# Kernel optimization log

Hardware: AMD Instinct MI355X
Metric: run time of the kernel (lower is better)

The kernel has to match this reference:

```python
import jax, jax.numpy as jnp
import numpy as np

B, T, D, H = 4, 2048, 1024, 16
HD = D // H  # head_dim = 64
MIX = 0.05   # cross-state coupling coefficient


def setup_inputs() -> dict:
    key = jax.random.key(0)
    ks = jax.random.split(key, 10)
    s = 0.02  # init scale for stability
    return {
        "x": jax.random.normal(ks[0], (B, T, D), jnp.float32),
        "Wq": jax.random.normal(ks[1], (D, D), jnp.float32) * s,
        "Wk": jax.random.normal(ks[2], (D, D), jnp.float32) * s,
        "Wv": jax.random.normal(ks[3], (D, D), jnp.float32) * s,
        "Wo": jax.random.normal(ks[4], (D, D), jnp.float32) * s,
        "Wb": jax.random.normal(ks[5], (H, D), jnp.float32) * s,
        "Wfd": jax.random.normal(ks[6], (H, D), jnp.float32) * s,
        "bfd": jnp.zeros((H,), jnp.float32),
        "Wsd": jax.random.normal(ks[7], (H, D), jnp.float32) * s,
        "bsd": jnp.zeros((H,), jnp.float32),
        "Wg": jax.random.normal(ks[8], (D, D), jnp.float32) * s,
    }


def _deltanet_forward(x, Wq, Wk, Wv, Wo, Wb, Wfd, bfd, Wsd, bsd, Wg):
    b, t, dm = x.shape
    # projections (nn.Linear: x @ W.T)
    def heads(W):  # [B,T,D] -> [B,H,T,hd]
        return (x @ W.T).reshape(b, t, H, HD).transpose(0, 2, 1, 3)
    q = jax.nn.silu(heads(Wq))
    k = jax.nn.silu(heads(Wk))
    v = jax.nn.silu(heads(Wv))
    beta = jax.nn.sigmoid(x @ Wb.T).transpose(0, 2, 1)               # [B,H,T]
    fd = jax.nn.sigmoid(x @ Wfd.T + bfd).transpose(0, 2, 1)          # [B,H,T]
    sd = jax.nn.sigmoid(x @ Wsd.T + bsd).transpose(0, 2, 1)          # [B,H,T]

    # time-major xs for scan
    qT = jnp.moveaxis(q, 2, 0)   # [T,B,H,hd]
    kT = jnp.moveaxis(k, 2, 0)
    vT = jnp.moveaxis(v, 2, 0)
    bT = jnp.moveaxis(beta, 2, 0)  # [T,B,H]
    fT = jnp.moveaxis(fd, 2, 0)
    sT = jnp.moveaxis(sd, 2, 0)

    def step(carry, inp):
        Sf, Ss = carry                       # each [B,H,hd]
        qt, kt, vt, bt, ft, st = inp
        Sf = Sf * ft[..., None]
        Ss = Ss * st[..., None]
        o = 0.5 * qt * (Sf + Ss)             # output before update
        upd = bt[..., None] * kt * vt
        Sf = Sf + upd
        Ss = Ss + upd
        Sf_new = Sf + MIX * Ss
        Ss = Ss + MIX * Sf                   # uses pre-mix Sf
        return (Sf_new, Ss), o

    S0 = jnp.zeros((b, H, HD), x.dtype)
    _, oT = jax.lax.scan(step, (S0, S0), (qT, kT, vT, bT, fT, sT))
    o = jnp.moveaxis(oT, 0, 2)               # [B,H,T,hd]
    o = o.transpose(0, 2, 1, 3).reshape(b, t, dm)  # [B,T,D]
    g = jax.nn.sigmoid(x @ Wg.T)
    return (o * g) @ Wo.T


def reference(x, Wq, Wk, Wv, Wo, Wb, Wfd, bfd, Wsd, bsd, Wg):
    return _deltanet_forward(x, Wq, Wk, Wv, Wo, Wb, Wfd, bfd, Wsd, bsd, Wg)
```

## Files before the change

### kernel.cpp

```cpp
#include <hip/hip_runtime.h>
#include <hip/hip_bf16.h>
#include <stdint.h>

#define BB 4
#define TT 2048
#define DD 1024
#define HH 16
#define MTOK (BB*TT)
#define NQ 4096
#define NW (NQ+128)
#define TC 32
#define NC (TT/TC)
#define BH (BB*HH)
#define ROWT (16*NQ)

typedef __bf16 bf16x8 __attribute__((ext_vector_type(8)));
typedef float f32x4 __attribute__((ext_vector_type(4)));

__device__ __forceinline__ uint16_t f2bf(float f){
  uint32_t u = __float_as_uint(f);
  u += 0x7fffu + ((u >> 16) & 1u);
  return (uint16_t)(u >> 16);
}
__device__ __forceinline__ float bf2f(uint32_t h){ return __uint_as_float(h << 16); }
__device__ __forceinline__ float sigm(float z){
  return __builtin_amdgcn_rcpf(1.f + __expf(-z));
}

__device__ __forceinline__ void gll16(const uint16_t* src, uint16_t* dst){
  __builtin_amdgcn_global_load_lds(
      (const __attribute__((address_space(1))) void*)src,
      (__attribute__((address_space(3))) void*)dst, 16, 0, 0);
}
__device__ __forceinline__ float bfel(const uint4& v, int e){
  uint32_t wrd = ((e>>1)==0) ? v.x : ((e>>1)==1) ? v.y : ((e>>1)==2) ? v.z : v.w;
  return bf2f((e&1) ? (wrd >> 16) : (wrd & 0xffffu));
}

__global__ __launch_bounds__(256) void prep_kernel(
    const float* __restrict__ x,
    const float* __restrict__ Wq, const float* __restrict__ Wk,
    const float* __restrict__ Wv, const float* __restrict__ Wg,
    const float* __restrict__ Wo,
    const float* __restrict__ Wb, const float* __restrict__ Wfd,
    const float* __restrict__ Wsd,
    uint16_t* __restrict__ wcat, uint16_t* __restrict__ wob,
    uint16_t* __restrict__ xb)
{
  const int bx = blockIdx.x;
  if (bx < 5120){
    int i = bx * 256 + threadIdx.x;
    int wsel = i >> 18;
    int loc = i & 262143;
    const float* src = (wsel == 0) ? Wq : (wsel == 1) ? Wk : (wsel == 2) ? Wv : (wsel == 3) ? Wg : Wo;
    uint16_t* dst = (wsel < 4) ? (wcat + (size_t)wsel * DD * DD) : wob;
    float4 v = ((const float4*)src)[loc];
    ushort4 o;
    o.x = f2bf(v.x); o.y = f2bf(v.y); o.z = f2bf(v.z); o.w = f2bf(v.w);
    ((ushort4*)dst)[loc] = o;
  } else if (bx < 9216){
    int base = (bx - 5120) * 512 + threadIdx.x;
    #pragma unroll
    for (int rep = 0; rep < 2; rep++){
      int loc = base + rep * 256;
      float4 v = ((const float4*)x)[loc];
      ushort4 o;
      o.x = f2bf(v.x); o.y = f2bf(v.y); o.z = f2bf(v.z); o.w = f2bf(v.w);
      ((ushort4*)xb)[loc] = o;
    }
  } else {
    int u = (bx - 9216) * 256 + threadIdx.x;
    int row = u >> 8;
    int cidx = (u & 255) * 4;
    ushort4 o = {0, 0, 0, 0};
    if (row < 48){
      const float* src = (row < 16) ? (Wb + (size_t)row * DD)
                       : (row < 32) ? (Wfd + (size_t)(row - 16) * DD)
                                    : (Wsd + (size_t)(row - 32) * DD);
      float4 v = *(const float4*)(src + cidx);
      o.x = f2bf(v.x); o.y = f2bf(v.y); o.z = f2bf(v.z); o.w = f2bf(v.w);
    }
    *(ushort4*)(wcat + (size_t)(NQ + row) * DD + cidx) = o;
  }
}

template<int MODE>
__global__ __launch_bounds__(256) void gemm128(
    const uint16_t* __restrict__ X, const uint16_t* __restrict__ W,
    uint16_t* __restrict__ Y, float* __restrict__ Yf,
    const float* __restrict__ bfd, const float* __restrict__ bsd,
    float* __restrict__ scp, int N, int K)
{
  __shared__ __align__(16) uint16_t lA[128 * 64];
  __shared__ __align__(16) uint16_t lB[128 * 64];
  const int tid = threadIdx.x;
  const int m0 = blockIdx.y * 128, n0 = blockIdx.x * 128;
  const int l = tid & 63, w = tid >> 6;
  const int wr = w >> 1, wc = w & 1;
  const int g = l >> 4, r16 = l & 15;

  const uint16_t* srcA[4];
  const uint16_t* srcB[4];
  uint16_t* dstA[4];
  uint16_t* dstB[4];
  #pragma unroll
  for (int n = 0; n < 4; n++){
    int p = n * 256 + tid;
    int row = p >> 3;
    int cq = (p & 7) ^ (row & 7);
    srcA[n] = X + (size_t)(m0 + row) * K + cq * 8;
    srcB[n] = W + (size_t)(n0 + row) * K + cq * 8;
    int basechunk = n * 256 + (tid & ~63);
    dstA[n] = lA + basechunk * 8;
    dstB[n] = lB + basechunk * 8;
  }

  int roA[4][2], roB[4][2];
  #pragma unroll
  for (int i = 0; i < 4; i++)
    #pragma unroll
    for (int ks = 0; ks < 2; ks++){
      roA[i][ks] = (wr * 64 + i * 16 + r16) * 64 + ((ks * 4 + g) ^ (r16 & 7)) * 8;
      roB[i][ks] = (wc * 64 + i * 16 + r16) * 64 + ((ks * 4 + g) ^ (r16 & 7)) * 8;
    }

  const bool doMfma = (MODE != 2) || (wc == 0);
  const int nLim = (MODE == 2) ? 3 : 4;

  f32x4 acc[4][4];
  #pragma unroll
  for (int i = 0; i < 4; i++)
    #pragma unroll
    for (int j = 0; j < 4; j++) acc[i][j] = (f32x4){0.f, 0.f, 0.f, 0.f};

  for (int kt = 0; kt < K; kt += 64){
    __syncthreads();
    #pragma unroll
    for (int n = 0; n < 4; n++){
      gll16(srcA[n] + kt, dstA[n]);
      gll16(srcB[n] + kt, dstB[n]);
    }
    __syncthreads();

    if (doMfma){
      #pragma unroll
      for (int ks = 0; ks < 2; ks++){
        bf16x8 af[4], bw[4];
        #pragma unroll
        for (int mi = 0; mi < 4; mi++) af[mi] = *(const bf16x8*)(lA + roA[mi][ks]);
        #pragma unroll
        for (int ni = 0; ni < nLim; ni++) bw[ni] = *(const bf16x8*)(lB + roB[ni][ks]);
        #pragma unroll
        for (int mi = 0; mi < 4; mi++)
          #pragma unroll
          for (int ni = 0; ni < nLim; ni++)
            acc[mi][ni] = __builtin_amdgcn_mfma_f32_16x16x32_bf16(af[mi], bw[ni], acc[mi][ni], 0, 0, 0);
      }
    }
  }

  if (MODE == 0){
    const bool dosig = (n0 >= 3 * DD);
    #pragma unroll
    for (int mi = 0; mi < 4; mi++){
      const int R0 = m0 + wr * 64 + mi * 16;
      const size_t rbase = (size_t)(R0 >> 4) * ROWT;
      #pragma unroll
      for (int ni = 0; ni < 4; ni++){
        const int C0 = n0 + wc * 64 + ni * 16;
        f32x4 v = acc[mi][ni];
        float o[4];
        #pragma unroll
        for (int r = 0; r < 4; r++){
          float xx = v[r];
          o[r] = dosig ? sigm(xx) : xx * sigm(xx);
        }
        uint2 pk;
        pk.x = (uint32_t)f2bf(o[0]) | ((uint32_t)f2bf(o[1]) << 16);
        pk.y = (uint32_t)f2bf(o[2]) | ((uint32_t)f2bf(o[3]) << 16);
        size_t off = rbase + (size_t)(C0 >> 4) * 256 + (size_t)r16 * 16 + g * 4;
        *(uint2*)(Y + off) = pk;
      }
    }
  } else if (MODE == 1){
    #pragma unroll
    for (int mi = 0; mi < 4; mi++){
      #pragma unroll
      for (int ni = 0; ni < 4; ni++){
        int rg = m0 + wr * 64 + mi * 16 + g * 4;
        int cg = n0 + wc * 64 + ni * 16 + r16;
        #pragma unroll
        for (int r = 0; r < 4; r++)
          Yf[(size_t)(rg + r) * N + cg] = acc[mi][ni][r];
      }
    }
  } else {
    if (wc == 0){
      #pragma unroll
      for (int ni = 0; ni < 3; ni++){
        const int grp = ni;
        const int h = r16;
        const float bias = (grp == 0) ? 0.f : (grp == 1) ? bfd[h] : bsd[h];
        #pragma unroll
        for (int mi = 0; mi < 4; mi++){
          const int R0 = m0 + wr * 64 + mi * 16 + g * 4;
          const int b = R0 >> 11, t = R0 & (TT - 1);
          f32x4 v = acc[mi][ni];
          float4 o;
          o.x = sigm(v[0] + bias);
          o.y = sigm(v[1] + bias);
          o.z = sigm(v[2] + bias);
          o.w = sigm(v[3] + bias);
          *(float4*)(scp + (((size_t)grp * BB + b) * HH + h) * TT + t) = o;
        }
      }
    }
  }
}


__global__ __launch_bounds__(64) void scan_partA(
    const uint16_t* __restrict__ qkvg, const float* __restrict__ sc,
    float* __restrict__ Lst, float4* __restrict__ Pm)
{
  int j = blockIdx.x, bh = blockIdx.y;
  int b = bh >> 4, h = bh & 15;
  int c = threadIdx.x;
  const int ci = c & 15;
  const size_t tc_k = (size_t)((DD     + h * 64 + c) >> 4) * 256 + ci * 16;
  const size_t tc_v = (size_t)((2 * DD + h * 64 + c) >> 4) * 256 + ci * 16;
  const float* bet = sc + ((size_t)(0 * BB + b) * HH + h) * TT + j * TC;
  const float* fdp = sc + ((size_t)(1 * BB + b) * HH + h) * TT + j * TC;
  const float* sdp = sc + ((size_t)(2 * BB + b) * HH + h) * TT + j * TC;

  float sf = 0.f, ss = 0.f;
  float p00 = 1.f, p01 = 0.f, p10 = 0.f, p11 = 1.f;
  #pragma unroll
  for (int t16 = 0; t16 < 2; ++t16){
    int R0 = b * TT + j * TC + t16 * 16;
    size_t tb = (size_t)(R0 >> 4) * ROWT;
    uint4 kl = *(const uint4*)(qkvg + tb + tc_k);
    uint4 kh = *(const uint4*)(qkvg + tb + tc_k + 8);
    uint4 vl = *(const uint4*)(qkvg + tb + tc_v);
    uint4 vh = *(const uint4*)(qkvg + tb + tc_v + 8);
    const float* bt = bet + t16 * 16;
    const float* ft = fdp + t16 * 16;
    const float* st = sdp + t16 * 16;
    #pragma unroll
    for (int u = 0; u < 16; ++u){
      float kv = (u < 8) ? bfel(kl, u) : bfel(kh, u - 8);
      float vv = (u < 8) ? bfel(vl, u) : bfel(vh, u - 8);
      float btv = bt[u], f = ft[u], s = st[u];
      float uu = 1.05f * btv * kv * vv;
      float bq = 0.05f * s, cq = 0.05f * f;
      float nf = f * sf + bq * ss + uu;
      float ns = cq * sf + s * ss + uu;
      sf = nf; ss = ns;
      float q00 = f * p00 + bq * p10, q01 = f * p01 + bq * p11;
      float q10 = cq * p00 + s * p10, q11 = cq * p01 + s * p11;
      p00 = q00; p01 = q01; p10 = q10; p11 = q11;
    }
  }
  size_t base = ((size_t)bh * NC + j) * 2;
  Lst[(base + 0) * 64 + c] = sf;
  Lst[(base + 1) * 64 + c] = ss;
  if (c == 0) Pm[(size_t)bh * NC + j] = make_float4(p00, p01, p10, p11);
}

__global__ __launch_bounds__(64) void scan_partC(
    const uint16_t* __restrict__ qkvg, const float* __restrict__ sc,
    const float* __restrict__ Lst, const float4* __restrict__ Pm,
    uint16_t* __restrict__ og)
{
  __shared__ uint16_t ot[16 * 64];
  int j = blockIdx.x, bh = blockIdx.y;
  int b = bh >> 4, h = bh & 15;
  int c = threadIdx.x;
  const int ci = c & 15;

  float sf = 0.f, ss = 0.f;
  for (int i = 0; i < j; ++i){
    size_t pbase = ((size_t)bh * NC + i) * 2;
    float lf = Lst[(pbase + 0) * 64 + c];
    float ls = Lst[(pbase + 1) * 64 + c];
    float4 P = Pm[(size_t)bh * NC + i];
    float nf = P.x * sf + P.y * ss + lf;
    float ns = P.z * sf + P.w * ss + ls;
    sf = nf; ss = ns;
  }

  const size_t tc_q = (size_t)((         h * 64 + c) >> 4) * 256 + ci * 16;
  const size_t tc_k = (size_t)((DD     + h * 64 + c) >> 4) * 256 + ci * 16;
  const size_t tc_v = (size_t)((2 * DD + h * 64 + c) >> 4) * 256 + ci * 16;
  const size_t tc_g = (size_t)((3 * DD + h * 64 + c) >> 4) * 256 + ci * 16;
  const float* bet = sc + ((size_t)(0 * BB + b) * HH + h) * TT + j * TC;
  const float* fdp = sc + ((size_t)(1 * BB + b) * HH + h) * TT + j * TC;
  const float* sdp = sc + ((size_t)(2 * BB + b) * HH + h) * TT + j * TC;

  #pragma unroll
  for (int t16 = 0; t16 < 2; ++t16){
    int R0 = b * TT + j * TC + t16 * 16;
    size_t tb = (size_t)(R0 >> 4) * ROWT;
    uint4 ql = *(const uint4*)(qkvg + tb + tc_q);
    uint4 qh = *(const uint4*)(qkvg + tb + tc_q + 8);
    uint4 kl = *(const uint4*)(qkvg + tb + tc_k);
    uint4 kh = *(const uint4*)(qkvg + tb + tc_k + 8);
    uint4 vl = *(const uint4*)(qkvg + tb + tc_v);
    uint4 vh = *(const uint4*)(qkvg + tb + tc_v + 8);
    uint4 gl = *(const uint4*)(qkvg + tb + tc_g);
    uint4 gh = *(const uint4*)(qkvg + tb + tc_g + 8);
    const float* bt = bet + t16 * 16;
    const float* ft = fdp + t16 * 16;
    const float* st = sdp + t16 * 16;
    #pragma unroll
    for (int u = 0; u < 16; ++u){
      float qv = (u < 8) ? bfel(ql, u) : bfel(qh, u - 8);
      float kv = (u < 8) ? bfel(kl, u) : bfel(kh, u - 8);
      float vv = (u < 8) ? bfel(vl, u) : bfel(vh, u - 8);
      float gv = (u < 8) ? bfel(gl, u) : bfel(gh, u - 8);
      float btv = bt[u], f = ft[u], s = st[u];
      sf *= f; ss *= s;
      float o = 0.5f * qv * (sf + ss);
      float uu = btv * kv * vv;
      sf += uu; ss += uu;
      float nf = sf + 0.05f * ss, ns = ss + 0.05f * sf;
      sf = nf; ss = ns;
      ot[u * 64 + c] = f2bf(o * gv);
    }
    __syncthreads();
    {
      int u0 = c >> 3, c8 = c & 7;
      uint4 d0 = *(const uint4*)&ot[u0 * 64 + c8 * 8];
      uint4 d1 = *(const uint4*)&ot[(u0 + 8) * 64 + c8 * 8];
      uint16_t* ob = og + (size_t)R0 * DD + h * 64 + c8 * 8;
      *(uint4*)(ob + (size_t)u0 * DD) = d0;
      *(uint4*)(ob + (size_t)(u0 + 8) * DD) = d1;
    }
    __syncthreads();
  }
}

extern "C" void kernel_launch(void* const* d_in, const int* in_sizes, int n_in,
                              void* d_out, int out_size, void* d_ws, size_t ws_size,
                              hipStream_t stream)
{
  const float* x   = (const float*)d_in[0];
  const float* Wq  = (const float*)d_in[1];
  const float* Wk  = (const float*)d_in[2];
  const float* Wv  = (const float*)d_in[3];
  const float* Wo  = (const float*)d_in[4];
  const float* Wb  = (const float*)d_in[5];
  const float* Wfd = (const float*)d_in[6];
  const float* bfd = (const float*)d_in[7];
  const float* Wsd = (const float*)d_in[8];
  const float* bsd = (const float*)d_in[9];
  const float* Wg  = (const float*)d_in[10];
  float* out = (float*)d_out;

  char* ws = (char*)d_ws;
  size_t off = 0;
  auto alloc = [&](size_t bytes) -> void* {
    void* p = ws + off;
    off += (bytes + 255) & ~(size_t)255;
    return p;
  };

  uint16_t* xb   = (uint16_t*)alloc((size_t)MTOK * DD * 2);
  uint16_t* wcat = (uint16_t*)alloc((size_t)NW * DD * 2);
  uint16_t* wob  = (uint16_t*)alloc((size_t)DD * DD * 2);
  uint16_t* qkvg = (uint16_t*)alloc((size_t)MTOK * NQ * 2);
  float*    sc   = (float*)alloc((size_t)3 * BB * HH * TT * 4);
  float*    Lst  = (float*)alloc((size_t)BH * NC * 2 * 64 * 4);
  float4*   Pm   = (float4*)alloc((size_t)BH * NC * 16);
  uint16_t* ogb  = xb;

  prep_kernel<<<9344, 256, 0, stream>>>(
      x, Wq, Wk, Wv, Wg, Wo, Wb, Wfd, Wsd, wcat, wob, xb);

  dim3 gp(1, MTOK / 128);
  gemm128<2><<<gp, 256, 0, stream>>>(xb, wcat + (size_t)NQ * DD, nullptr, nullptr,
                                     bfd, bsd, sc, NQ, DD);

  dim3 gq(NQ / 128, MTOK / 128);
  gemm128<0><<<gq, 256, 0, stream>>>(xb, wcat, qkvg, nullptr, bfd, bsd, nullptr, NQ, DD);

  dim3 gs(NC, BH);
  scan_partA<<<gs, 64, 0, stream>>>(qkvg, sc, Lst, Pm);
  scan_partC<<<gs, 64, 0, stream>>>(qkvg, sc, Lst, Pm, ogb);

  dim3 go(DD / 128, MTOK / 128);
  gemm128<1><<<go, 256, 0, stream>>>(ogb, wob, nullptr, out, bfd, bsd, nullptr, DD, DD);
}
```

Baseline: 170.8 us.

## Replace QKVG projection GEMM with 256x256-tile, 8-wave, double-buffered pipelined kernel

Adds a dedicated QKVG GEMM kernel using 256x256 output tiles with 512 threads and an 8x4 MFMA accumulator tile per wave. The K loop double-buffers LDS via direct global-to-LDS loads, splits each k-step into half-tiles interleaved with barriers, and raises wave priority around the MFMA bursts so loads overlap compute. This targets the largest GEMM (8192x4096x1024) by improving operand reuse and hiding load latency. The cost is heavy register pressure (128 accumulator floats per lane) and 128 KB of LDS per block, which limits occupancy. Only 512 blocks are launched, so the wave count across the device is small.

```diff
diff --git a/kernel.cpp b/kernel.cpp
--- a/kernel.cpp
+++ b/kernel.cpp
@@ -84,6 +84,155 @@
   }
 }
 
+__global__ __launch_bounds__(512, 2) void gemm256_qkvg(
+    const uint16_t* __restrict__ X, const uint16_t* __restrict__ W,
+    uint16_t* __restrict__ Y)
+{
+  constexpr int K = DD;
+  constexpr int NT = K / 64;
+  constexpr int HSZ = 8192;
+  __shared__ __align__(16) uint16_t sA[2][2][HSZ];
+  __shared__ __align__(16) uint16_t sB[2][2][HSZ];
+
+  const int tid = threadIdx.x;
+  const int m0 = blockIdx.y * 256, n0 = blockIdx.x * 256;
+  const int l = tid & 63, w = tid >> 6;
+  const int wr = w >> 2, wc = w & 3;
+  const int g = l >> 4, r16 = l & 15;
+
+  const int c1 = tid + 512;
+  const int r0 = tid >> 2, q0 = (tid & 3) ^ ((tid >> 3) & 3);
+  const int r1 = c1 >> 2,  q1 = (c1 & 3) ^ ((c1 >> 3) & 3);
+  const uint16_t* pA0 = X + (size_t)(m0 + r0) * K + q0 * 8;
+  const uint16_t* pA1 = X + (size_t)(m0 + r1) * K + q1 * 8;
+  const uint16_t* pB0 = W + (size_t)(n0 + r0) * K + q0 * 8;
+  const uint16_t* pB1 = W + (size_t)(n0 + r1) * K + q1 * 8;
+  const int d0 = w * 512, d1 = 4096 + w * 512;
+
+  const int fsw = (g ^ ((r16 >> 1) & 3)) * 8;
+  int roA[8], roB[4];
+  #pragma unroll
+  for (int mi = 0; mi < 8; mi++) roA[mi] = (wr * 128 + mi * 16 + r16) * 32 + fsw;
+  #pragma unroll
+  for (int ni = 0; ni < 4; ni++) roB[ni] = (wc * 64 + ni * 16 + r16) * 32 + fsw;
+
+  f32x4 acc[8][4];
+  #pragma unroll
+  for (int i = 0; i < 8; i++)
+    #pragma unroll
+    for (int j = 0; j < 4; j++) acc[i][j] = (f32x4){0.f, 0.f, 0.f, 0.f};
+
+  gll16(pA0,      &sA[0][0][d0]); gll16(pA1,      &sA[0][0][d1]);
+  gll16(pB0,      &sB[0][0][d0]); gll16(pB1,      &sB[0][0][d1]);
+  gll16(pA0 + 32, &sA[0][1][d0]); gll16(pA1 + 32, &sA[0][1][d1]);
+  gll16(pB0 + 32, &sB[0][1][d0]); gll16(pB1 + 32, &sB[0][1][d1]);
+  asm volatile("s_waitcnt vmcnt(4)" ::: "memory");
+  __builtin_amdgcn_sched_barrier(0);
+  __builtin_amdgcn_s_barrier();
+
+  #pragma unroll 1
+  for (int t = 0; t < NT; ++t){
+    const int buf = t & 1, nb = buf ^ 1;
+    const bool st = (t + 1 < NT);
+    const int kof = (t + 1) * 64;
+    bf16x8 a[8], b0, b1, b2, b3;
+
+    #pragma unroll
+    for (int mi = 0; mi < 8; mi++) a[mi] = *(const bf16x8*)&sA[buf][0][roA[mi]];
+    b0 = *(const bf16x8*)&sB[buf][0][roB[0]];
+    b1 = *(const bf16x8*)&sB[buf][0][roB[1]];
+    if (st){ gll16(pA0 + kof, &sA[nb][0][d0]); gll16(pA1 + kof, &sA[nb][0][d1]); }
+    __builtin_amdgcn_s_barrier();
+    asm volatile("s_waitcnt lgkmcnt(0)" ::: "memory");
+    __builtin_amdgcn_sched_barrier(0);
+    __builtin_amdgcn_s_setprio(1);
+    #pragma unroll
+    for (int mi = 0; mi < 8; mi++){
+      acc[mi][0] = __builtin_amdgcn_mfma_f32_16x16x32_bf16(a[mi], b0, acc[mi][0], 0, 0, 0);
+      acc[mi][1] = __builtin_amdgcn_mfma_f32_16x16x32_bf16(a[mi], b1, acc[mi][1], 0, 0, 0);
+    }
+    __builtin_amdgcn_s_setprio(0);
+    __builtin_amdgcn_s_barrier();
+
+    b2 = *(const bf16x8*)&sB[buf][0][roB[2]];
+    b3 = *(const bf16x8*)&sB[buf][0][roB[3]];
+    if (st){ gll16(pB0 + kof, &sB[nb][0][d0]); gll16(pB1 + kof, &sB[nb][0][d1]); }
+    __builtin_amdgcn_s_barrier();
+    asm volatile("s_waitcnt lgkmcnt(0)" ::: "memory");
+    __builtin_amdgcn_sched_barrier(0);
+    __builtin_amdgcn_s_setprio(1);
+    #pragma unroll
+    for (int mi = 0; mi < 8; mi++){
+      acc[mi][2] = __builtin_amdgcn_mfma_f32_16x16x32_bf16(a[mi], b2, acc[mi][2], 0, 0, 0);
+      acc[mi][3] = __builtin_amdgcn_mfma_f32_16x16x32_bf16(a[mi], b3, acc[mi][3], 0, 0, 0);
+    }
+    __builtin_amdgcn_s_setprio(0);
+    if (st) asm volatile("s_waitcnt vmcnt(4)" ::: "memory");
+    else    asm volatile("s_waitcnt vmcnt(0)" ::: "memory");
+    __builtin_amdgcn_sched_barrier(0);
+    __builtin_amdgcn_s_barrier();
+
+    #pragma unroll
+    for (int mi = 0; mi < 8; mi++) a[mi] = *(const bf16x8*)&sA[buf][1][roA[mi]];
+    b0 = *(const bf16x8*)&sB[buf][1][roB[0]];
+    b1 = *(const bf16x8*)&sB[buf][1][roB[1]];
+    if (st){ gll16(pA0 + kof + 32, &sA[nb][1][d0]); gll16(pA1 + kof + 32, &sA[nb][1][d1]); }
+    __builtin_amdgcn_s_barrier();
+    asm volatile("s_waitcnt lgkmcnt(0)" ::: "memory");
+    __builtin_amdgcn_sched_barrier(0);
+    __builtin_amdgcn_s_setprio(1);
+    #pragma unroll
+    for (int mi = 0; mi < 8; mi++){
+      acc[mi][0] = __builtin_amdgcn_mfma_f32_16x16x32_bf16(a[mi], b0, acc[mi][0], 0, 0, 0);
+      acc[mi][1] = __builtin_amdgcn_mfma_f32_16x16x32_bf16(a[mi], b1, acc[mi][1], 0, 0, 0);
+    }
+    __builtin_amdgcn_s_setprio(0);
+    __builtin_amdgcn_s_barrier();
+
+    b2 = *(const bf16x8*)&sB[buf][1][roB[2]];
+    b3 = *(const bf16x8*)&sB[buf][1][roB[3]];
+    if (st){ gll16(pB0 + kof + 32, &sB[nb][1][d0]); gll16(pB1 + kof + 32, &sB[nb][1][d1]); }
+    __builtin_amdgcn_s_barrier();
+    asm volatile("s_waitcnt lgkmcnt(0)" ::: "memory");
+    __builtin_amdgcn_sched_barrier(0);
+    __builtin_amdgcn_s_setprio(1);
+    #pragma unroll
+    for (int mi = 0; mi < 8; mi++){
+      acc[mi][2] = __builtin_amdgcn_mfma_f32_16x16x32_bf16(a[mi], b2, acc[mi][2], 0, 0, 0);
+      acc[mi][3] = __builtin_amdgcn_mfma_f32_16x16x32_bf16(a[mi], b3, acc[mi][3], 0, 0, 0);
+    }
+    __builtin_amdgcn_s_setprio(0);
+    if (st){
+      asm volatile("s_waitcnt vmcnt(4)" ::: "memory");
+      __builtin_amdgcn_sched_barrier(0);
+      __builtin_amdgcn_s_barrier();
+    }
+  }
+
+  const bool dosig = (n0 >= 3 * DD);
+  #pragma unroll
+  for (int mi = 0; mi < 8; ++mi){
+    const int R0 = m0 + wr * 128 + mi * 16;
+    const size_t rbase = (size_t)(R0 >> 4) * ROWT;
+    #pragma unroll
+    for (int ni = 0; ni < 4; ++ni){
+      const int C0 = n0 + wc * 64 + ni * 16;
+      f32x4 v = acc[mi][ni];
+      float o[4];
+      #pragma unroll
+      for (int r = 0; r < 4; r++){
+        float xx = v[r];
+        o[r] = dosig ? sigm(xx) : xx * sigm(xx);
+      }
+      uint2 pk;
+      pk.x = (uint32_t)f2bf(o[0]) | ((uint32_t)f2bf(o[1]) << 16);
+      pk.y = (uint32_t)f2bf(o[2]) | ((uint32_t)f2bf(o[3]) << 16);
+      size_t off = rbase + (size_t)(C0 >> 4) * 256 + (size_t)r16 * 16 + g * 4;
+      *(uint2*)(Y + off) = pk;
+    }
+  }
+}
+
 template<int MODE>
 __global__ __launch_bounds__(256) void gemm128(
     const uint16_t* __restrict__ X, const uint16_t* __restrict__ W,
@@ -159,30 +308,7 @@
     }
   }
 
-  if (MODE == 0){
-    const bool dosig = (n0 >= 3 * DD);
-    #pragma unroll
-    for (int mi = 0; mi < 4; mi++){
-      const int R0 = m0 + wr * 64 + mi * 16;
-      const size_t rbase = (size_t)(R0 >> 4) * ROWT;
-      #pragma unroll
-      for (int ni = 0; ni < 4; ni++){
-        const int C0 = n0 + wc * 64 + ni * 16;
-        f32x4 v = acc[mi][ni];
-        float o[4];
-        #pragma unroll
-        for (int r = 0; r < 4; r++){
-          float xx = v[r];
-          o[r] = dosig ? sigm(xx) : xx * sigm(xx);
-        }
-        uint2 pk;
-        pk.x = (uint32_t)f2bf(o[0]) | ((uint32_t)f2bf(o[1]) << 16);
-        pk.y = (uint32_t)f2bf(o[2]) | ((uint32_t)f2bf(o[3]) << 16);
-        size_t off = rbase + (size_t)(C0 >> 4) * 256 + (size_t)r16 * 16 + g * 4;
-        *(uint2*)(Y + off) = pk;
-      }
-    }
-  } else if (MODE == 1){
+  if (MODE == 1){
     #pragma unroll
     for (int mi = 0; mi < 4; mi++){
       #pragma unroll
@@ -218,7 +344,6 @@
   }
 }
 
-
 __global__ __launch_bounds__(64) void scan_partA(
     const uint16_t* __restrict__ qkvg, const float* __restrict__ sc,
     float* __restrict__ Lst, float4* __restrict__ Pm)
@@ -381,8 +506,8 @@
   gemm128<2><<<gp, 256, 0, stream>>>(xb, wcat + (size_t)NQ * DD, nullptr, nullptr,
                                      bfd, bsd, sc, NQ, DD);
 
-  dim3 gq(NQ / 128, MTOK / 128);
-  gemm128<0><<<gq, 256, 0, stream>>>(xb, wcat, qkvg, nullptr, bfd, bsd, nullptr, NQ, DD);
+  dim3 gq(NQ / 256, MTOK / 256);
+  gemm256_qkvg<<<gq, 512, 0, stream>>>(xb, wcat, qkvg);
 
   dim3 gs(NC, BH);
   scan_partA<<<gs, 64, 0, stream>>>(qkvg, sc, Lst, Pm);
```

Result: faster. 163.1 us (-4.5%).
